# Optimization experiments

Hardware: AMD Instinct MI355X
Metric: run time of the kernel (lower is better)

Reference implementation:

```python
import jax, jax.numpy as jnp
import numpy as np

B, S, E = 256, 128, 1024


def setup_inputs() -> dict:
    key = jax.random.key(0)
    k1, k2, k3, k4, k5 = jax.random.split(key, 5)
    x = jax.random.normal(k1, (B, S, E), dtype=jnp.float32)
    # ragged bags: start in [0,32), length in [1,96] so end <= 128 and bags are non-empty
    starts = jax.random.randint(k2, (B,), 0, 32)
    lengths = jax.random.randint(k3, (B,), 1, 97)
    document_index = jnp.stack([starts, starts + lengths], axis=-1).astype(jnp.int32)  # [B,2]
    scale = 1.0 / np.sqrt(E)
    W = jax.random.normal(k4, (E, E), dtype=jnp.float32) * scale  # relationMatrix.weight
    u = jax.random.normal(k5, (1, E), dtype=jnp.float32) * scale  # relationVector.weight
    return {"x": x, "W": W, "u": u, "document_index": document_index}


def reference(x, W, u, document_index):
    # scores_bs = relationVector(tanh(relationMatrix(x)))  (bias-free linears)
    h = jnp.tanh(jnp.einsum('bse,fe->bsf', x, W))          # [B,S,E]
    scores = jnp.einsum('bse,e->bs', h, u[0])              # [B,S]
    # ragged mask: position s belongs to doc b iff start <= s < end
    idx = jnp.arange(S)[None, :]                            # [1,S]
    mask = (idx >= document_index[:, :1]) & (idx < document_index[:, 1:])  # [B,S]
    attn = jax.nn.softmax(jnp.where(mask, scores, -jnp.inf), axis=-1)      # [B,S]
    attn = jnp.where(mask, attn, 0.0)
    out_concat = jnp.einsum('bs,bse->be', attn, x)          # [B,E]
    # keep_attention in the original is the last bag's softmax weights;
    # here returned padded to length S (zeros outside the bag)
    keep_attention = attn[-1]                               # [S]
    return out_concat, keep_attention
```

## Files before the change

kernel.cpp:

```cpp
#include <hip/hip_runtime.h>
#include <math.h>

#define Bb 256
#define Ss 128
#define Ee 1024
#define BK 64
#define APAD 72

typedef __bf16 bf16x8 __attribute__((ext_vector_type(8)));
typedef float f32x4 __attribute__((ext_vector_type(4)));

typedef __attribute__((address_space(3))) unsigned int lds_u32;
typedef __attribute__((address_space(1))) unsigned int glb_u32;

static __device__ __forceinline__ unsigned short f2bf(float f) {
    unsigned int u = __float_as_uint(f);
    u += 0x7FFFu + ((u >> 16) & 1u);
    return (unsigned short)(u >> 16);
}
static __device__ __forceinline__ float bf2f(unsigned short h) {
    return __uint_as_float((unsigned int)h << 16);
}

__global__ void conv_all(const float* __restrict__ x,
                         const float* __restrict__ W,
                         const int* __restrict__ doc,
                         unsigned short* __restrict__ xb,
                         unsigned short* __restrict__ Wb) {
    const int st = blockIdx.x, by = blockIdx.y, tid = threadIdx.x;
    if (by >= Bb) {
        int i = ((((by - Bb) << 3) | st) << 8) | tid;
        float4 v = reinterpret_cast<const float4*>(W)[i];
        ushort4 o;
        o.x = f2bf(v.x); o.y = f2bf(v.y); o.z = f2bf(v.z); o.w = f2bf(v.w);
        reinterpret_cast<ushort4*>(Wb)[i] = o;
        return;
    }
    const int b = by;
    const int start = doc[2 * b], end = doc[2 * b + 1];
    const int strip0 = start >> 4;
    const int ns = ((end + 15) >> 4) - strip0;
    if (st < strip0 || st >= strip0 + ns) return;
    const size_t base = ((size_t)b * Ss + (st << 4)) * Ee;
    #pragma unroll
    for (int r = 0; r < 16; ++r) {
        size_t idx = base + (size_t)r * Ee + (tid << 2);
        float4 v = *reinterpret_cast<const float4*>(x + idx);
        ushort4 o;
        o.x = f2bf(v.x); o.y = f2bf(v.y); o.z = f2bf(v.z); o.w = f2bf(v.w);
        *reinterpret_cast<ushort4*>(xb + idx) = o;
    }
}

__global__ void convW_kernel(const float* __restrict__ W, unsigned short* __restrict__ Wb) {
    int i = blockIdx.x * blockDim.x + threadIdx.x;
    float4 v = reinterpret_cast<const float4*>(W)[i];
    ushort4 o;
    o.x = f2bf(v.x); o.y = f2bf(v.y); o.z = f2bf(v.z); o.w = f2bf(v.w);
    reinterpret_cast<ushort4*>(Wb)[i] = o;
}

__launch_bounds__(256, 6)
__global__ void scores_gemm_xb(const unsigned short* __restrict__ xb,
                               const unsigned short* __restrict__ Wb,
                               const float* __restrict__ u,
                               const int* __restrict__ doc,
                               float* __restrict__ part) {
    __shared__ __align__(16) unsigned short As[64 * BK];
    __shared__ __align__(16) unsigned short Bs[128 * BK];
    __shared__ float s_red[4][64];

    const int b  = blockIdx.x;
    const int ft = blockIdx.y;
    const int mh = blockIdx.z;
    const int start = doc[2 * b], end = doc[2 * b + 1];
    const int strip0 = start >> 4;
    const int ns = ((end + 15) >> 4) - strip0;
    const int ms0 = mh << 2;
    if (ms0 >= ns) return;
    const int nsl = min(ns - ms0, 4);
    const int row0 = (strip0 + ms0) << 4;
    const int na = nsl << 7;

    const int tid  = threadIdx.x;
    const int wave = tid >> 6;
    const int lane = tid & 63;
    const int quad = lane >> 4;
    const int l16  = lane & 15;

    const unsigned short* abase = xb + ((size_t)b * Ss + row0) * Ee;
    const unsigned short* wbase = Wb + (size_t)ft * 128 * Ee;

    f32x4 acc[4][2];
    #pragma unroll
    for (int i = 0; i < 4; ++i)
        #pragma unroll
        for (int j = 0; j < 2; ++j) acc[i][j] = (f32x4){0.f, 0.f, 0.f, 0.f};

    for (int t = 0; t < 16; ++t) {
        const int k0 = t << 6;
        #pragma unroll
        for (int r = 0; r < 2; ++r) {
            int chunk = (r << 8) | tid;
            if (chunk < na) {
                int arow = chunk >> 3;
                int c8 = (chunk & 7) ^ (arow & 7);
                __builtin_amdgcn_global_load_lds(
                    (const glb_u32*)(abase + (size_t)arow * Ee + k0 + (c8 << 3)),
                    (lds_u32*)&As[chunk << 3], 16, 0, 0);
            }
        }
        #pragma unroll
        for (int r = 0; r < 4; ++r) {
            int chunk = (r << 8) | tid;
            int brow = chunk >> 3;
            int c8 = (chunk & 7) ^ (brow & 7);
            __builtin_amdgcn_global_load_lds(
                (const glb_u32*)(wbase + (size_t)brow * Ee + k0 + (c8 << 3)),
                (lds_u32*)&Bs[chunk << 3], 16, 0, 0);
        }
        __syncthreads();

        #pragma unroll
        for (int kk = 0; kk < BK; kk += 32) {
            const int n0 = wave * 32 + l16;
            const int n1 = n0 + 16;
            const int c8k = (kk >> 3) + quad;
            bf16x8 bf0 = *reinterpret_cast<const bf16x8*>(
                &Bs[((n0 << 3) | (c8k ^ (n0 & 7))) << 3]);
            bf16x8 bf1 = *reinterpret_cast<const bf16x8*>(
                &Bs[((n1 << 3) | (c8k ^ (n1 & 7))) << 3]);
            #pragma unroll
            for (int st = 0; st < 4; ++st) {
                if (st < nsl) {
                    const int ar = st * 16 + l16;
                    bf16x8 af = *reinterpret_cast<const bf16x8*>(
                        &As[((ar << 3) | (c8k ^ (ar & 7))) << 3]);
                    acc[st][0] = __builtin_amdgcn_mfma_f32_16x16x32_bf16(af, bf0, acc[st][0], 0, 0, 0);
                    acc[st][1] = __builtin_amdgcn_mfma_f32_16x16x32_bf16(af, bf1, acc[st][1], 0, 0, 0);
                }
            }
        }
        __syncthreads();
    }

    const float u0 = u[ft * 128 + wave * 32 + l16];
    const float u1 = u[ft * 128 + wave * 32 + 16 + l16];
    #pragma unroll
    for (int st = 0; st < 4; ++st) {
        if (st < nsl) {
            float p[4];
            #pragma unroll
            for (int r = 0; r < 4; ++r)
                p[r] = tanhf(acc[st][0][r]) * u0 + tanhf(acc[st][1][r]) * u1;
            #pragma unroll
            for (int off = 8; off >= 1; off >>= 1)
                #pragma unroll
                for (int r = 0; r < 4; ++r)
                    p[r] += __shfl_xor(p[r], off, 16);
            if (l16 == 0)
                #pragma unroll
                for (int r = 0; r < 4; ++r)
                    s_red[wave][st * 16 + quad * 4 + r] = p[r];
        }
    }
    __syncthreads();
    if (tid < (nsl << 4)) {
        float v = s_red[0][tid] + s_red[1][tid] + s_red[2][tid] + s_red[3][tid];
        part[((size_t)(b * Ss + row0 + tid) << 3) | ft] = v;
    }
}

__launch_bounds__(256)
__global__ void scores_gemm_fb(const float* __restrict__ x,
                               const unsigned short* __restrict__ Wb,
                               const float* __restrict__ u,
                               const int* __restrict__ doc,
                               float* __restrict__ part) {
    __shared__ __align__(16) unsigned short As[8 * 16 * APAD];
    __shared__ __align__(16) unsigned short Bs[128 * BK];
    __shared__ float s_red[4][128];

    const int b  = blockIdx.x;
    const int ft = blockIdx.y;
    const int start = doc[2 * b], end = doc[2 * b + 1];
    const int strip0 = start >> 4;
    const int ns = ((end + 15) >> 4) - strip0;
    const int row0 = strip0 << 4;

    const int tid  = threadIdx.x;
    const int wave = tid >> 6;
    const int lane = tid & 63;
    const int quad = lane >> 4;
    const int l16  = lane & 15;
    const int arow = tid >> 4;
    const int acol = (tid & 15) << 2;

    const float* xbase = x + ((size_t)b * Ss + row0) * Ee;
    const unsigned short* wbase = Wb + (size_t)ft * 128 * Ee;

    f32x4 acc[8][2];
    #pragma unroll
    for (int i = 0; i < 8; ++i)
        #pragma unroll
        for (int j = 0; j < 2; ++j) acc[i][j] = (f32x4){0.f, 0.f, 0.f, 0.f};

    for (int k0 = 0; k0 < Ee; k0 += BK) {
        #pragma unroll
        for (int r = 0; r < 8; ++r) if (r < ns) {
            int row = (r << 4) | arow;
            float4 v = *reinterpret_cast<const float4*>(xbase + (size_t)row * Ee + k0 + acol);
            ushort4 o; o.x = f2bf(v.x); o.y = f2bf(v.y); o.z = f2bf(v.z); o.w = f2bf(v.w);
            *reinterpret_cast<ushort4*>(&As[row * APAD + acol]) = o;
        }
        #pragma unroll
        for (int r = 0; r < 4; ++r) {
            int chunk = (r << 8) | tid;
            int brow = chunk >> 3;
            int c8 = (chunk & 7) ^ (brow & 7);
            __builtin_amdgcn_global_load_lds(
                (const glb_u32*)(wbase + (size_t)brow * Ee + k0 + (c8 << 3)),
                (lds_u32*)&Bs[chunk << 3], 16, 0, 0);
        }
        __syncthreads();
        #pragma unroll
        for (int kk = 0; kk < BK; kk += 32) {
            const int n0 = wave * 32 + l16;
            const int n1 = n0 + 16;
            const int c8k = (kk >> 3) + quad;
            bf16x8 bf0 = *reinterpret_cast<const bf16x8*>(
                &Bs[((n0 << 3) | (c8k ^ (n0 & 7))) << 3]);
            bf16x8 bf1 = *reinterpret_cast<const bf16x8*>(
                &Bs[((n1 << 3) | (c8k ^ (n1 & 7))) << 3]);
            #pragma unroll
            for (int st = 0; st < 8; ++st) {
                if (st < ns) {
                    bf16x8 af = *reinterpret_cast<const bf16x8*>(
                        &As[(st * 16 + l16) * APAD + kk + quad * 8]);
                    acc[st][0] = __builtin_amdgcn_mfma_f32_16x16x32_bf16(af, bf0, acc[st][0], 0, 0, 0);
                    acc[st][1] = __builtin_amdgcn_mfma_f32_16x16x32_bf16(af, bf1, acc[st][1], 0, 0, 0);
                }
            }
        }
        __syncthreads();
    }

    const float u0 = u[ft * 128 + wave * 32 + l16];
    const float u1 = u[ft * 128 + wave * 32 + 16 + l16];
    #pragma unroll
    for (int st = 0; st < 8; ++st) {
        if (st < ns) {
            float p[4];
            #pragma unroll
            for (int r = 0; r < 4; ++r)
                p[r] = tanhf(acc[st][0][r]) * u0 + tanhf(acc[st][1][r]) * u1;
            #pragma unroll
            for (int off = 8; off >= 1; off >>= 1)
                #pragma unroll
                for (int r = 0; r < 4; ++r)
                    p[r] += __shfl_xor(p[r], off, 16);
            if (l16 == 0)
                #pragma unroll
                for (int r = 0; r < 4; ++r)
                    s_red[wave][st * 16 + quad * 4 + r] = p[r];
        }
    }
    __syncthreads();
    if (tid < (ns << 4)) {
        float v = s_red[0][tid] + s_red[1][tid] + s_red[2][tid] + s_red[3][tid];
        part[((size_t)(b * Ss + row0 + tid) << 3) | ft] = v;
    }
}

__global__ void out_fused(const unsigned short* __restrict__ xb,
                          const float* __restrict__ x,
                          const float* __restrict__ part,
                          const int* __restrict__ doc,
                          float* __restrict__ out,
                          float* __restrict__ keep) {
    const int c = blockIdx.x, b = blockIdx.y, t = threadIdx.x;
    const int start = doc[2 * b], end = doc[2 * b + 1];
    __shared__ float a_s[Ss];
    __shared__ float red[2];

    bool m = false;
    float sc = -INFINITY;
    if (t < Ss) {
        m = (t >= start) && (t < end);
        if (m) {
            const float4* p = reinterpret_cast<const float4*>(part + ((size_t)(b * Ss + t) << 3));
            float4 p0 = p[0], p1 = p[1];
            sc = ((p0.x + p0.y) + (p0.z + p0.w)) + ((p1.x + p1.y) + (p1.z + p1.w));
        }
    }
    float v = sc;
    #pragma unroll
    for (int off = 32; off >= 1; off >>= 1)
        v = fmaxf(v, __shfl_xor(v, off, 64));
    if (t < Ss && (t & 63) == 0) red[t >> 6] = v;
    __syncthreads();
    const float mx = fmaxf(red[0], red[1]);
    __syncthreads();
    const float e = m ? __expf(sc - mx) : 0.f;
    v = e;
    #pragma unroll
    for (int off = 32; off >= 1; off >>= 1)
        v += __shfl_xor(v, off, 64);
    if (t < Ss && (t & 63) == 0) red[t >> 6] = v;
    __syncthreads();
    if (t < Ss) a_s[t] = e / (red[0] + red[1]);
    __syncthreads();
    if (b == Bb - 1 && c == 0 && t < Ss) keep[t] = a_s[t];

    const int slo = max(start, c << 5), shi = min(end, (c << 5) + 32);
    if (slo >= shi) return;

    float4 accv = {0.f, 0.f, 0.f, 0.f};
    if (xb) {
        const unsigned short* xr = xb + (size_t)b * Ss * Ee;
        for (int s = slo; s < shi; ++s) {
            float a = a_s[s];
            ushort4 q = *reinterpret_cast<const ushort4*>(xr + (size_t)s * Ee + (t << 2));
            accv.x += a * bf2f(q.x); accv.y += a * bf2f(q.y);
            accv.z += a * bf2f(q.z); accv.w += a * bf2f(q.w);
        }
    } else {
        const float4* xr = reinterpret_cast<const float4*>(x + (size_t)b * Ss * Ee);
        for (int s = slo; s < shi; ++s) {
            float a = a_s[s];
            float4 q = xr[s * 256 + t];
            accv.x += a * q.x; accv.y += a * q.y;
            accv.z += a * q.z; accv.w += a * q.w;
        }
    }
    float* o = out + (size_t)b * Ee + (t << 2);
    atomicAdd(o + 0, accv.x);
    atomicAdd(o + 1, accv.y);
    atomicAdd(o + 2, accv.z);
    atomicAdd(o + 3, accv.w);
}

extern "C" void kernel_launch(void* const* d_in, const int* in_sizes, int n_in,
                              void* d_out, int out_size, void* d_ws, size_t ws_size,
                              hipStream_t stream) {
    const float* x  = (const float*)d_in[0];
    const float* W  = (const float*)d_in[1];
    const float* u  = (const float*)d_in[2];
    const int* doc  = (const int*)d_in[3];
    float* out = (float*)d_out;

    const size_t szWb   = (size_t)Ee * Ee * 2;
    const size_t szXb   = (size_t)Bb * Ss * Ee * 2;
    const size_t szPart = (size_t)Bb * Ss * 8 * 4;

    unsigned short* Wb = (unsigned short*)d_ws;
    const bool big_ws = ws_size >= szWb + szXb + szPart;

    hipMemsetAsync(out, 0, (size_t)Bb * Ee * sizeof(float), stream);

    if (big_ws) {
        unsigned short* xbuf = (unsigned short*)((char*)d_ws + szWb);
        float* part = (float*)((char*)d_ws + szWb + szXb);
        conv_all<<<dim3(8, Bb + 128), 256, 0, stream>>>(x, W, doc, xbuf, Wb);
        scores_gemm_xb<<<dim3(Bb, 8, 2), 256, 0, stream>>>(xbuf, Wb, u, doc, part);
        out_fused<<<dim3(4, Bb), 256, 0, stream>>>(xbuf, x, part, doc, out, out + (size_t)Bb * Ee);
    } else {
        float* part = (float*)((char*)d_ws + szWb);
        convW_kernel<<<1024, 256, 0, stream>>>(W, Wb);
        scores_gemm_fb<<<dim3(Bb, 8), 256, 0, stream>>>(x, Wb, u, doc, part);
        out_fused<<<dim3(4, Bb), 256, 0, stream>>>(nullptr, x, part, doc, out, out + (size_t)Bb * Ee);
    }
}
```

Before: 280.1 us.

## Pack valid 16-row strips across documents into dense GEMM tiles

Adds a prefix-sum kernel that builds a compacted list of all active 16-row strips across all bags. The scores GEMM then iterates over packed groups of four strips, so every block fills its 64-row tile instead of running partially empty or early-exiting blocks per bag. This aims to raise MFMA utilization and cut idle blocks, at the cost of an extra tiny launch, gathered row loads from different bags, and padding that recomputes duplicate strips in the tail.

```diff
diff --git a/kernel.cpp b/kernel.cpp
--- a/kernel.cpp
+++ b/kernel.cpp
@@ -6,6 +6,7 @@
 #define Ee 1024
 #define BK 64
 #define APAD 72
+#define NMAX 2048
 
 typedef __bf16 bf16x8 __attribute__((ext_vector_type(8)));
 typedef float f32x4 __attribute__((ext_vector_type(4)));
@@ -20,6 +21,29 @@
 }
 static __device__ __forceinline__ float bf2f(unsigned short h) {
     return __uint_as_float((unsigned int)h << 16);
+}
+
+__global__ void build_list(const int* __restrict__ doc, int* __restrict__ list) {
+    __shared__ int sc[256];
+    const int b = threadIdx.x;
+    const int start = doc[2 * b], end = doc[2 * b + 1];
+    const int s0 = start >> 4;
+    const int ns = ((end + 15) >> 4) - s0;
+    sc[b] = ns;
+    __syncthreads();
+    for (int d = 1; d < 256; d <<= 1) {
+        int v = sc[b];
+        int add = (b >= d) ? sc[b - d] : 0;
+        __syncthreads();
+        sc[b] = v + add;
+        __syncthreads();
+    }
+    const int total = sc[255];
+    const int off = sc[b] - ns;
+    for (int i = 0; i < ns; ++i)
+        list[off + i] = b * Ss + ((s0 + i) << 4);
+    for (int i = total + b; i < NMAX; i += 256)
+        list[i] = -1;
 }
 
 __global__ void conv_all(const float* __restrict__ x,
@@ -64,23 +88,26 @@
 __global__ void scores_gemm_xb(const unsigned short* __restrict__ xb,
                                const unsigned short* __restrict__ Wb,
                                const float* __restrict__ u,
-                               const int* __restrict__ doc,
+                               const int* __restrict__ list,
                                float* __restrict__ part) {
     __shared__ __align__(16) unsigned short As[64 * BK];
     __shared__ __align__(16) unsigned short Bs[128 * BK];
     __shared__ float s_red[4][64];
 
-    const int b  = blockIdx.x;
+    const int mb = blockIdx.x;
     const int ft = blockIdx.y;
-    const int mh = blockIdx.z;
-    const int start = doc[2 * b], end = doc[2 * b + 1];
-    const int strip0 = start >> 4;
-    const int ns = ((end + 15) >> 4) - strip0;
-    const int ms0 = mh << 2;
-    if (ms0 >= ns) return;
-    const int nsl = min(ns - ms0, 4);
-    const int row0 = (strip0 + ms0) << 4;
-    const int na = nsl << 7;
+
+    int e0 = list[mb << 2];
+    if (e0 < 0) return;
+    int e[4];
+    bool val[4];
+    e[0] = e0; val[0] = true;
+    #pragma unroll
+    for (int j = 1; j < 4; ++j) {
+        int v = list[(mb << 2) | j];
+        val[j] = v >= 0;
+        e[j] = val[j] ? v : e0;
+    }
 
     const int tid  = threadIdx.x;
     const int wave = tid >> 6;
@@ -88,7 +115,6 @@
     const int quad = lane >> 4;
     const int l16  = lane & 15;
 
-    const unsigned short* abase = xb + ((size_t)b * Ss + row0) * Ee;
     const unsigned short* wbase = Wb + (size_t)ft * 128 * Ee;
 
     f32x4 acc[4][2];
@@ -102,13 +128,13 @@
         #pragma unroll
         for (int r = 0; r < 2; ++r) {
             int chunk = (r << 8) | tid;
-            if (chunk < na) {
-                int arow = chunk >> 3;
-                int c8 = (chunk & 7) ^ (arow & 7);
-                __builtin_amdgcn_global_load_lds(
-                    (const glb_u32*)(abase + (size_t)arow * Ee + k0 + (c8 << 3)),
-                    (lds_u32*)&As[chunk << 3], 16, 0, 0);
-            }
+            int arow = chunk >> 3;
+            int strip = arow >> 4;
+            int rowin = arow & 15;
+            int c8 = (chunk & 7) ^ (arow & 7);
+            __builtin_amdgcn_global_load_lds(
+                (const glb_u32*)(xb + ((size_t)e[strip] + rowin) * Ee + k0 + (c8 << 3)),
+                (lds_u32*)&As[chunk << 3], 16, 0, 0);
         }
         #pragma unroll
         for (int r = 0; r < 4; ++r) {
@@ -132,13 +158,11 @@
                 &Bs[((n1 << 3) | (c8k ^ (n1 & 7))) << 3]);
             #pragma unroll
             for (int st = 0; st < 4; ++st) {
-                if (st < nsl) {
-                    const int ar = st * 16 + l16;
-                    bf16x8 af = *reinterpret_cast<const bf16x8*>(
-                        &As[((ar << 3) | (c8k ^ (ar & 7))) << 3]);
-                    acc[st][0] = __builtin_amdgcn_mfma_f32_16x16x32_bf16(af, bf0, acc[st][0], 0, 0, 0);
-                    acc[st][1] = __builtin_amdgcn_mfma_f32_16x16x32_bf16(af, bf1, acc[st][1], 0, 0, 0);
-                }
+                const int ar = st * 16 + l16;
+                bf16x8 af = *reinterpret_cast<const bf16x8*>(
+                    &As[((ar << 3) | (c8k ^ (ar & 7))) << 3]);
+                acc[st][0] = __builtin_amdgcn_mfma_f32_16x16x32_bf16(af, bf0, acc[st][0], 0, 0, 0);
+                acc[st][1] = __builtin_amdgcn_mfma_f32_16x16x32_bf16(af, bf1, acc[st][1], 0, 0, 0);
             }
         }
         __syncthreads();
@@ -148,26 +172,27 @@
     const float u1 = u[ft * 128 + wave * 32 + 16 + l16];
     #pragma unroll
     for (int st = 0; st < 4; ++st) {
-        if (st < nsl) {
-            float p[4];
+        float p[4];
+        #pragma unroll
+        for (int r = 0; r < 4; ++r)
+            p[r] = tanhf(acc[st][0][r]) * u0 + tanhf(acc[st][1][r]) * u1;
+        #pragma unroll
+        for (int off = 8; off >= 1; off >>= 1)
             #pragma unroll
             for (int r = 0; r < 4; ++r)
-                p[r] = tanhf(acc[st][0][r]) * u0 + tanhf(acc[st][1][r]) * u1;
-            #pragma unroll
-            for (int off = 8; off >= 1; off >>= 1)
-                #pragma unroll
-                for (int r = 0; r < 4; ++r)
-                    p[r] += __shfl_xor(p[r], off, 16);
-            if (l16 == 0)
-                #pragma unroll
-                for (int r = 0; r < 4; ++r)
-                    s_red[wave][st * 16 + quad * 4 + r] = p[r];
-        }
-    }
-    __syncthreads();
-    if (tid < (nsl << 4)) {
-        float v = s_red[0][tid] + s_red[1][tid] + s_red[2][tid] + s_red[3][tid];
-        part[((size_t)(b * Ss + row0 + tid) << 3) | ft] = v;
+                p[r] += __shfl_xor(p[r], off, 16);
+        if (l16 == 0)
+            #pragma unroll
+            for (int r = 0; r < 4; ++r)
+                s_red[wave][st * 16 + quad * 4 + r] = p[r];
+    }
+    __syncthreads();
+    if (tid < 64) {
+        const int strip = tid >> 4;
+        if (val[strip]) {
+            float v = s_red[0][tid] + s_red[1][tid] + s_red[2][tid] + s_red[3][tid];
+            part[((size_t)(e[strip] + (tid & 15)) << 3) | ft] = v;
+        }
     }
 }
 
@@ -352,17 +377,20 @@
     const size_t szWb   = (size_t)Ee * Ee * 2;
     const size_t szXb   = (size_t)Bb * Ss * Ee * 2;
     const size_t szPart = (size_t)Bb * Ss * 8 * 4;
+    const size_t szList = (size_t)NMAX * 4;
 
     unsigned short* Wb = (unsigned short*)d_ws;
-    const bool big_ws = ws_size >= szWb + szXb + szPart;
+    const bool big_ws = ws_size >= szWb + szXb + szPart + szList;
 
     hipMemsetAsync(out, 0, (size_t)Bb * Ee * sizeof(float), stream);
 
     if (big_ws) {
         unsigned short* xbuf = (unsigned short*)((char*)d_ws + szWb);
         float* part = (float*)((char*)d_ws + szWb + szXb);
+        int* list = (int*)((char*)d_ws + szWb + szXb + szPart);
+        build_list<<<1, 256, 0, stream>>>(doc, list);
         conv_all<<<dim3(8, Bb + 128), 256, 0, stream>>>(x, W, doc, xbuf, Wb);
-        scores_gemm_xb<<<dim3(Bb, 8, 2), 256, 0, stream>>>(xbuf, Wb, u, doc, part);
+        scores_gemm_xb<<<dim3(NMAX / 4, 8), 256, 0, stream>>>(xbuf, Wb, u, list, part);
         out_fused<<<dim3(4, Bb), 256, 0, stream>>>(xbuf, x, part, doc, out, out + (size_t)Bb * Ee);
     } else {
         float* part = (float*)((char*)d_ws + szWb);
```

New measurement: 261.4 us. 6.7% less time.
